# Kernel optimization log

Measured on AMD Instinct MI355X. Metric: run time of the kernel, lower is better.

The kernel has to match this reference:

```python
import jax, jax.numpy as jnp
import numpy as np
from jax import lax

PAD = 1  # 3x3 conv, stride 1, padding 1


def conv2d(x, w, b=None):
    # x: [B,C,H,W], w: [O,I,3,3]
    y = lax.conv_general_dilated(x, w, window_strides=(1, 1),
                                 padding=((PAD, PAD), (PAD, PAD)),
                                 dimension_numbers=("NCHW", "OIHW", "NCHW"))
    if b is not None:
        y = y + b[None, :, None, None]
    return y


def _bilinear(img, py, px):
    # img: [C,H,W]; py,px: [K,H,W] sampling coords (float). Zero padding outside.
    H, W = img.shape[1], img.shape[2]
    y0 = jnp.floor(py)
    x0 = jnp.floor(px)
    wy = py - y0  # [K,H,W]
    wx = px - x0
    y0i = y0.astype(jnp.int32)
    x0i = x0.astype(jnp.int32)

    def gather(yi, xi):
        valid = ((yi >= 0) & (yi < H) & (xi >= 0) & (xi < W)).astype(img.dtype)
        yc = jnp.clip(yi, 0, H - 1)
        xc = jnp.clip(xi, 0, W - 1)
        return img[:, yc, xc] * valid[None]  # [C,K,H,W]

    v00 = gather(y0i, x0i)
    v01 = gather(y0i, x0i + 1)
    v10 = gather(y0i + 1, x0i)
    v11 = gather(y0i + 1, x0i + 1)
    return (v00 * (1 - wy) * (1 - wx) + v01 * (1 - wy) * wx
            + v10 * wy * (1 - wx) + v11 * wy * wx)  # [C,K,H,W]


def reference(x, w_offset, b_offset, w_mask, b_mask, w_conv):
    B, C, H, W = x.shape
    K = 9  # 3x3 kernel taps
    offset = conv2d(x, w_offset, b_offset)              # [B,2K,H,W]
    mask = jax.nn.sigmoid(conv2d(x, w_mask, b_mask))    # [B,K,H,W]

    off = offset.reshape(B, K, 2, H, W)
    dy = off[:, :, 0]  # [B,K,H,W] (torchvision layout: y first)
    dx = off[:, :, 1]

    k = jnp.arange(K)
    ky = (k // 3).astype(x.dtype) - PAD  # tap row offset in {-1,0,1}
    kx = (k % 3).astype(x.dtype) - PAD
    ii = jnp.arange(H, dtype=x.dtype)
    jj = jnp.arange(W, dtype=x.dtype)

    py = ii[None, None, :, None] + ky[None, :, None, None] + dy  # [B,K,H,W]
    px = jj[None, None, None, :] + kx[None, :, None, None] + dx

    sampled = jax.vmap(_bilinear)(x, py, px)  # [B,C,K,H,W]
    sampled = sampled * mask[:, None]          # modulated deform-conv v2

    # weight [64,3,3,3] -> [O,C,K]; contract over C and kernel taps
    out = jnp.einsum('bckhw,ock->bohw', sampled, w_conv.reshape(w_conv.shape[0], C, K))
    return out


def setup_inputs() -> dict:
    key = jax.random.key(0)
    k = jax.random.split(key, 6)
    B, C, H, W = 16, 3, 256, 256
    return {
        'x': jax.random.normal(k[0], (B, C, H, W), jnp.float32),
        'w_offset': jax.random.normal(k[1], (18, 3, 3, 3), jnp.float32) * 0.1,
        'b_offset': jax.random.normal(k[2], (18,), jnp.float32) * 0.1,
        'w_mask': jax.random.normal(k[3], (9, 3, 3, 3), jnp.float32) * 0.1,
        'b_mask': jax.random.normal(k[4], (9,), jnp.float32) * 0.1,
        'w_conv': jax.random.normal(k[5], (64, 3, 3, 3), jnp.float32) * 0.1,
    }
```

## Files before the change

kernel.cpp:

```cpp
#include <hip/hip_runtime.h>
#include <hip/hip_bf16.h>

#define HH 256
#define WW 256
#define CC 3
#define KK 9
#define OC 64
#define KD 27
#define PSTS 40
#define MOFF 5120
#define MST 16
#define WRB 6144
#define XST (4 * WRB)
#define XSLOT 1024
#define ROWS 4
#define SLOTS 10

typedef __attribute__((ext_vector_type(8))) short bf16x8;
typedef __attribute__((ext_vector_type(4))) short s16x4;
typedef __attribute__((ext_vector_type(4))) float f32x4;
typedef __attribute__((ext_vector_type(2))) float f32x2;
typedef __attribute__((ext_vector_type(2))) unsigned int u32x2;

static __device__ __forceinline__ short f2bf(float f) {
    __hip_bfloat16 h = __float2bfloat16(f);
    return __builtin_bit_cast(short, h);
}
static __device__ __forceinline__ unsigned pack2(short a, short b) {
    return (unsigned)(unsigned short)a | ((unsigned)(unsigned short)b << 16);
}
static __device__ __forceinline__ float bf2f(unsigned w) {
    return __uint_as_float(w << 16);
}
static __device__ __forceinline__ float bfup(unsigned w) {
    return __uint_as_float(w & 0xffff0000u);
}

__global__ __launch_bounds__(256) void dcn_prep(
    const float* __restrict__ x,
    const float* __restrict__ w_offset, const float* __restrict__ b_offset,
    const float* __restrict__ w_mask,   const float* __restrict__ b_mask,
    const float* __restrict__ w_conv,
    short* __restrict__ xbf, short* __restrict__ wcf, char* __restrict__ wof,
    int npix)
{
    const int tid = threadIdx.x;
    if (blockIdx.x == gridDim.x - 1) {
        if (tid < 64) {
            const int fm = tid & 15, kc = tid >> 4;
#pragma unroll
            for (int t = 0; t < 4; ++t) {
                bf16x8 v;
#pragma unroll
                for (int e = 0; e < 8; ++e) {
                    int kd = kc * 8 + e;
                    v[e] = (kd < KD) ? f2bf(w_conv[(t * 16 + fm) * KD + kd]) : (short)0;
                }
                *(bf16x8*)(wcf + tid * 32 + t * 8) = v;
            }
#pragma unroll
            for (int t = 0; t < 2; ++t) {
                int ch = t * 16 + fm;
                bf16x8 vh, vl;
#pragma unroll
                for (int e = 0; e < 8; ++e) {
                    int kd = kc * 8 + e;
                    float val = 0.0f;
                    if (kd < KD) {
                        if (ch < 18) val = w_offset[ch * KD + kd];
                        else if (ch < KD) val = w_mask[(ch - 18) * KD + kd];
                    }
                    unsigned u = __float_as_uint(val);
                    vh[e] = (short)(u >> 16);
                    float d = val - __uint_as_float(u & 0xffff0000u);
                    vl[e] = (short)(__float_as_uint(d) >> 16);
                }
                *(bf16x8*)(wof + tid * 96 + t * 16) = vh;
                *(bf16x8*)(wof + tid * 96 + 32 + t * 16) = vl;
            }
#pragma unroll
            for (int t = 0; t < 2; ++t) {
                f32x4 cb;
#pragma unroll
                for (int r = 0; r < 4; ++r) {
                    int ch = t * 16 + kc * 4 + r;
                    float v = 0.0f;
                    if (ch < 18) v = b_offset[ch];
                    else if (ch < KD) v = b_mask[ch - 18];
                    cb[r] = v;
                }
                *(f32x4*)(wof + tid * 96 + 64 + t * 16) = cb;
            }
        }
        return;
    }

    const int p0 = (blockIdx.x * 256 + tid) * 4;
    if (p0 >= npix) return;
    const int bb = p0 >> 16;
    const int q  = p0 & 0xffff;
    const float* xb = x + (size_t)bb * (3 * 65536) + q;
    f32x4 r0 = *(const f32x4*)(xb);
    f32x4 r1 = *(const f32x4*)(xb + 65536);
    f32x4 r2 = *(const f32x4*)(xb + 131072);

    bf16x8 v0 = {f2bf(r0[0]), f2bf(r1[0]), f2bf(r2[0]), 0,
                 f2bf(r0[1]), f2bf(r1[1]), f2bf(r2[1]), 0};
    bf16x8 v1 = {f2bf(r0[2]), f2bf(r1[2]), f2bf(r2[2]), 0,
                 f2bf(r0[3]), f2bf(r1[3]), f2bf(r2[3]), 0};
    short* A = xbf + (size_t)p0 * 4;
    *(bf16x8*)A       = v0;
    *(bf16x8*)(A + 8) = v1;
}

__global__ __launch_bounds__(256) void dcn_main(
    const float* __restrict__ x,
    const short* __restrict__ xbf,
    const short* __restrict__ wcf,
    const char*  __restrict__ wof,
    float* __restrict__ out)
{
    __shared__ __align__(16) char LDSBUF[XST + SLOTS * XSLOT * 2];

    const int tid = threadIdx.x;
    const int j = tid;
    const int r0 = (blockIdx.x & 63) * ROWS;
    const int b = blockIdx.x >> 6;
    const int lane = tid & 63;
    const int wv = tid >> 6;
    const int fm = lane & 15;
    const int kc = lane >> 4;

    char* wbase = LDSBUF + wv * WRB;
    short* patchS = (short*)wbase;
    short* xs = (short*)(LDSBUF + XST);

    const float* xb = x + (size_t)b * (CC * HH * WW);
    const short* xrow = xbf + (size_t)b * (HH * WW * 4);

    {
        u32x2 st[SLOTS];
#pragma unroll
        for (int s = 0; s < SLOTS; ++s) {
            int gr = min(max(r0 - 3 + s, 0), HH - 1);
            st[s] = *(const u32x2*)(xrow + ((size_t)gr * WW + tid) * 4);
        }
#pragma unroll
        for (int s = 0; s < SLOTS; ++s) {
            *(u32x2*)(xs + s * XSLOT + tid * 4) = st[s];
        }
    }
    __syncthreads();

    const char* wl = wof + lane * 96;
    bf16x8 whi0 = *(const bf16x8*)(wl);
    bf16x8 whi1 = *(const bf16x8*)(wl + 16);
    bf16x8 wlo0 = *(const bf16x8*)(wl + 32);
    bf16x8 wlo1 = *(const bf16x8*)(wl + 48);
    f32x4 cb0 = *(const f32x4*)(wl + 64);
    f32x4 cb1 = *(const f32x4*)(wl + 80);
    bf16x8 afrag[4];
#pragma unroll
    for (int t2 = 0; t2 < 4; ++t2) afrag[t2] = *(const bf16x8*)(wcf + lane * 32 + t2 * 8);

    const float* x0p = xb;
    const float* x1p = xb + (size_t)HH * WW;
    const float* x2p = xb + (size_t)2 * HH * WW;

#pragma unroll 1
    for (int d = 0; d < ROWS; ++d) {
        const int ri = r0 + d;

        const bool yok0 = (ri - 1) >= 0, yok2 = (ri + 1) < HH;
        const bool xok0 = (j - 1) >= 0, xok2 = (j + 1) < WW;
        s16x4 pr[3][3];
#pragma unroll
        for (int p = 0; p < 3; ++p) {
#pragma unroll
            for (int q = 0; q < 3; ++q) {
                int xx = min(max(j + q - 1, 0), WW - 1);
                pr[p][q] = *(const s16x4*)(xs + (d + p + 2) * XSLOT + xx * 4);
            }
        }
        {
            short* rp = patchS + lane * PSTS;
#pragma unroll
            for (int o = 0; o < 4; ++o) {
                bf16x8 vh;
#pragma unroll
                for (int e = 0; e < 8; ++e) {
                    int kd = o * 8 + e;
                    if (kd < KD) {
                        int c = kd / 9, rem = kd - c * 9, p = rem / 3, q = rem - p * 3;
                        bool ok = (p == 0 ? yok0 : (p == 2 ? yok2 : true)) &&
                                  (q == 0 ? xok0 : (q == 2 ? xok2 : true));
                        vh[e] = ok ? pr[p][q][c] : (short)0;
                    } else {
                        vh[e] = (short)0;
                    }
                }
                *(bf16x8*)(rp + o * 8) = vh;
            }
        }

        f32x4 dacc[4][2];
#pragma unroll
        for (int g = 0; g < 4; ++g) {
            bf16x8 phi = *(const bf16x8*)(patchS + (g * 16 + fm) * PSTS + kc * 8);
            f32x4 a0 = __builtin_amdgcn_mfma_f32_16x16x32_bf16(whi0, phi, cb0, 0, 0, 0);
            a0 = __builtin_amdgcn_mfma_f32_16x16x32_bf16(wlo0, phi, a0, 0, 0, 0);
            f32x4 a1 = __builtin_amdgcn_mfma_f32_16x16x32_bf16(whi1, phi, cb1, 0, 0, 0);
            a1 = __builtin_amdgcn_mfma_f32_16x16x32_bf16(wlo1, phi, a1, 0, 0, 0);
            dacc[g][0] = a0;
            dacc[g][1] = a1;
        }
#pragma unroll
        for (int g = 0; g < 4; ++g) {
            int r = g * 16 + fm;
            char* dr = wbase + r * 80;
            char* mr = wbase + MOFF + r * MST;
            *(f32x4*)(dr + kc * 16) = dacc[g][0];
            f32x4 a1 = dacc[g][1];
            if (kc == 0) {
                *(f32x2*)(dr + 64) = (f32x2){a1[0], a1[1]};
                *(unsigned*)(dr + 72) = pack2(f2bf(a1[2]), f2bf(a1[3]));
            } else if (kc == 1) {
                *(unsigned*)(dr + 76) = pack2(f2bf(a1[0]), f2bf(a1[1]));
                *(unsigned*)(mr + 0) = pack2(f2bf(a1[2]), f2bf(a1[3]));
            } else if (kc == 2) {
                *(unsigned*)(mr + 4) = pack2(f2bf(a1[0]), f2bf(a1[1]));
                *(unsigned short*)(mr + 8) = (unsigned short)f2bf(a1[2]);
            }
        }

        const char* myD = wbase + lane * 80;
        f32x4 d03 = *(const f32x4*)(myD);
        f32x4 d47 = *(const f32x4*)(myD + 16);
        f32x4 d8b = *(const f32x4*)(myD + 32);
        f32x4 dcf = *(const f32x4*)(myD + 48);
        f32x2 d8p = *(const f32x2*)(myD + 64);
        u32x2 z03 = *(const u32x2*)(myD + 72);
        const char* myM = wbase + MOFF + lane * MST;
        u32x2 z47 = *(const u32x2*)(myM);
        unsigned z8w = *(const unsigned short*)(myM + 8);

        const float dyv[9] = {d03[0], d03[2], d47[0], d47[2], d8b[0], d8b[2], dcf[0], dcf[2], d8p[0]};
        const float dxv[9] = {d03[1], d03[3], d47[1], d47[3], d8b[1], d8b[3], dcf[1], dcf[3], d8p[1]};
        const float mzf[9] = {bf2f(z03.x), bfup(z03.x), bf2f(z03.y), bfup(z03.y),
                              bf2f(z47.x), bfup(z47.x), bf2f(z47.y), bfup(z47.y), bf2f(z8w)};

        float s27[KD];
#pragma unroll
        for (int k = 0; k < KK; ++k) {
            float dy = dyv[k], dx = dxv[k];
            float msk = 1.0f / (1.0f + __expf(-mzf[k]));

            float py = (float)(ri + (k / 3) - 1) + dy;
            float px = (float)(j + (k % 3) - 1) + dx;
            float y0f = floorf(py), x0f = floorf(px);
            float wy = py - y0f, wx = px - x0f;
            int y0 = (int)y0f, x0 = (int)x0f;
            int y1 = y0 + 1, x1 = x0 + 1;

            float w00 = (1.0f - wy) * (1.0f - wx);
            float w01 = (1.0f - wy) * wx;
            float w10 = wy * (1.0f - wx);
            float w11 = wy * wx;

            bool v0y = (unsigned)y0 < HH, v1y = (unsigned)y1 < HH;
            bool v0x = (unsigned)x0 < WW, v1x = (unsigned)x1 < WW;
            float f00 = (v0y && v0x) ? w00 : 0.0f;
            float f01 = (v0y && v1x) ? w01 : 0.0f;
            float f10 = (v1y && v0x) ? w10 : 0.0f;
            float f11 = (v1y && v1x) ? w11 : 0.0f;

            int y0c = min(max(y0, 0), HH - 1), y1c = min(max(y1, 0), HH - 1);
            int s0 = y0c - r0 + 3;
            int s1 = y1c - r0 + 3;
            float r0v_, r1v_, r2v_;
            if (__builtin_expect(__any(((unsigned)s0 > (SLOTS - 1)) ||
                                       ((unsigned)s1 > (SLOTS - 1))), 0)) {
                int x0c = min(max(x0, 0), WW - 1), x1c = min(max(x1, 0), WW - 1);
                int o00 = y0c * WW + x0c, o01 = y0c * WW + x1c;
                int o10 = y1c * WW + x0c, o11 = y1c * WW + x1c;
                r0v_ = x0p[o00] * f00 + x0p[o01] * f01 + x0p[o10] * f10 + x0p[o11] * f11;
                r1v_ = x1p[o00] * f00 + x1p[o01] * f01 + x1p[o10] * f10 + x1p[o11] * f11;
                r2v_ = x2p[o00] * f00 + x2p[o01] * f01 + x2p[o10] * f10 + x2p[o11] * f11;
            } else {
                int xl = min(max(x0, 0), WW - 2);
                bool sw = (x0 != xl);
                const short* p0 = xs + s0 * XSLOT + xl * 4;
                const short* p1 = xs + s1 * XSLOT + xl * 4;
                u32x2 lo0 = *(const u32x2*)p0;
                u32x2 hi0 = *(const u32x2*)(p0 + 4);
                u32x2 lo1 = *(const u32x2*)p1;
                u32x2 hi1 = *(const u32x2*)(p1 + 4);

                float a0 = sw ? f01 : f00, b0 = sw ? f00 : f01;
                float a1w = sw ? f11 : f10, b1w = sw ? f10 : f11;

                r0v_ = fmaf(bf2f(lo0.x), a0, fmaf(bf2f(hi0.x), b0,
                       fmaf(bf2f(lo1.x), a1w, bf2f(hi1.x) * b1w)));
                r1v_ = fmaf(bfup(lo0.x), a0, fmaf(bfup(hi0.x), b0,
                       fmaf(bfup(lo1.x), a1w, bfup(hi1.x) * b1w)));
                r2v_ = fmaf(bf2f(lo0.y), a0, fmaf(bf2f(hi0.y), b0,
                       fmaf(bf2f(lo1.y), a1w, bf2f(hi1.y) * b1w)));
            }
            s27[k]      = r0v_ * msk;
            s27[9 + k]  = r1v_ * msk;
            s27[18 + k] = r2v_ * msk;
        }

        {
            short* srow = patchS + lane * PSTS;
#pragma unroll
            for (int o = 0; o < 4; ++o) {
                bf16x8 v;
#pragma unroll
                for (int e = 0; e < 8; ++e) {
                    int kd = o * 8 + e;
                    v[e] = (kd < KD) ? f2bf(s27[kd]) : (short)0;
                }
                *(bf16x8*)(srow + o * 8) = v;
            }
        }

        float* obase = out + ((size_t)b * OC * HH + ri) * WW;
#pragma unroll
        for (int g = 0; g < 4; ++g) {
            bf16x8 sfrag = *(const bf16x8*)(patchS + (g * 16 + fm) * PSTS + kc * 8);
#pragma unroll
            for (int t2 = 0; t2 < 4; ++t2) {
                f32x4 acc = (f32x4){0.f, 0.f, 0.f, 0.f};
                acc = __builtin_amdgcn_mfma_f32_16x16x32_bf16(sfrag, afrag[t2], acc, 0, 0, 0);
                float* op = obase + (size_t)(t2 * 16 + fm) * (HH * WW) + (wv * 64 + g * 16 + kc * 4);
                *(f32x4*)op = acc;
            }
        }
    }
}

extern "C" void kernel_launch(void* const* d_in, const int* in_sizes, int n_in,
                              void* d_out, int out_size, void* d_ws, size_t ws_size,
                              hipStream_t stream) {
    const float* x        = (const float*)d_in[0];
    const float* w_offset = (const float*)d_in[1];
    const float* b_offset = (const float*)d_in[2];
    const float* w_mask   = (const float*)d_in[3];
    const float* b_mask   = (const float*)d_in[4];
    const float* w_conv   = (const float*)d_in[5];
    float* out = (float*)d_out;

    int B = in_sizes[0] / (CC * HH * WW);
    int npix = B * HH * WW;

    short* xbf = (short*)d_ws;
    short* wcf = (short*)((char*)d_ws + (size_t)npix * 8);
    char*  wof = (char*)d_ws + (size_t)npix * 8 + 4096;

    int nb = (npix + 1023) / 1024;
    hipLaunchKernelGGL(dcn_prep, dim3(nb + 1), dim3(256), 0, stream,
                       x, w_offset, b_offset, w_mask, b_mask, w_conv,
                       xbf, wcf, wof, npix);
    hipLaunchKernelGGL(dcn_main, dim3(B * (HH / ROWS)), dim3(256), 0, stream,
                       x, xbf, wcf, wof, out);
}
```

Measured before the change: 75.74 us.

## Shrink per-wave LDS, quantize mask to 8-bit, halve rows per block

```diff
diff --git a/kernel.cpp b/kernel.cpp
--- a/kernel.cpp
+++ b/kernel.cpp
@@ -8,19 +8,18 @@
 #define OC 64
 #define KD 27
 #define PSTS 40
-#define MOFF 5120
-#define MST 16
-#define WRB 6144
+#define WRB 5120
 #define XST (4 * WRB)
 #define XSLOT 1024
-#define ROWS 4
-#define SLOTS 10
+#define ROWS 2
+#define SLOTS 8
 
 typedef __attribute__((ext_vector_type(8))) short bf16x8;
 typedef __attribute__((ext_vector_type(4))) short s16x4;
 typedef __attribute__((ext_vector_type(4))) float f32x4;
 typedef __attribute__((ext_vector_type(2))) float f32x2;
 typedef __attribute__((ext_vector_type(2))) unsigned int u32x2;
+typedef __attribute__((ext_vector_type(4))) unsigned int u32x4;
 
 static __device__ __forceinline__ short f2bf(float f) {
     __hip_bfloat16 h = __float2bfloat16(f);
@@ -34,6 +33,10 @@
 }
 static __device__ __forceinline__ float bfup(unsigned w) {
     return __uint_as_float(w & 0xffff0000u);
+}
+static __device__ __forceinline__ unsigned q8(float z) {
+    float s = 1.0f / (1.0f + __expf(-z));
+    return (unsigned)__builtin_rintf(s * 255.0f);
 }
 
 __global__ __launch_bounds__(256) void dcn_prep(
@@ -113,7 +116,7 @@
     *(bf16x8*)(A + 8) = v1;
 }
 
-__global__ __launch_bounds__(256) void dcn_main(
+__global__ __launch_bounds__(256, 4) void dcn_main(
     const float* __restrict__ x,
     const short* __restrict__ xbf,
     const short* __restrict__ wcf,
@@ -124,8 +127,8 @@
 
     const int tid = threadIdx.x;
     const int j = tid;
-    const int r0 = (blockIdx.x & 63) * ROWS;
-    const int b = blockIdx.x >> 6;
+    const int r0 = (blockIdx.x & 127) * ROWS;
+    const int b = blockIdx.x >> 7;
     const int lane = tid & 63;
     const int wv = tid >> 6;
     const int fm = lane & 15;
@@ -218,18 +221,17 @@
         for (int g = 0; g < 4; ++g) {
             int r = g * 16 + fm;
             char* dr = wbase + r * 80;
-            char* mr = wbase + MOFF + r * MST;
             *(f32x4*)(dr + kc * 16) = dacc[g][0];
             f32x4 a1 = dacc[g][1];
             if (kc == 0) {
-                *(f32x2*)(dr + 64) = (f32x2){a1[0], a1[1]};
-                *(unsigned*)(dr + 72) = pack2(f2bf(a1[2]), f2bf(a1[3]));
+                *(unsigned*)(dr + 64) = pack2(f2bf(a1[0]), f2bf(a1[1]));
+                *(unsigned short*)(dr + 68) = (unsigned short)(q8(a1[2]) | (q8(a1[3]) << 8));
             } else if (kc == 1) {
-                *(unsigned*)(dr + 76) = pack2(f2bf(a1[0]), f2bf(a1[1]));
-                *(unsigned*)(mr + 0) = pack2(f2bf(a1[2]), f2bf(a1[3]));
+                *(unsigned short*)(dr + 70) = (unsigned short)(q8(a1[0]) | (q8(a1[1]) << 8));
+                *(unsigned short*)(dr + 72) = (unsigned short)(q8(a1[2]) | (q8(a1[3]) << 8));
             } else if (kc == 2) {
-                *(unsigned*)(mr + 4) = pack2(f2bf(a1[0]), f2bf(a1[1]));
-                *(unsigned short*)(mr + 8) = (unsigned short)f2bf(a1[2]);
+                *(unsigned short*)(dr + 74) = (unsigned short)(q8(a1[0]) | (q8(a1[1]) << 8));
+                *(unsigned short*)(dr + 76) = (unsigned short)q8(a1[2]);
             }
         }
 
@@ -238,22 +240,21 @@
         f32x4 d47 = *(const f32x4*)(myD + 16);
         f32x4 d8b = *(const f32x4*)(myD + 32);
         f32x4 dcf = *(const f32x4*)(myD + 48);
-        f32x2 d8p = *(const f32x2*)(myD + 64);
-        u32x2 z03 = *(const u32x2*)(myD + 72);
-        const char* myM = wbase + MOFF + lane * MST;
-        u32x2 z47 = *(const u32x2*)(myM);
-        unsigned z8w = *(const unsigned short*)(myM + 8);
-
-        const float dyv[9] = {d03[0], d03[2], d47[0], d47[2], d8b[0], d8b[2], dcf[0], dcf[2], d8p[0]};
-        const float dxv[9] = {d03[1], d03[3], d47[1], d47[3], d8b[1], d8b[3], dcf[1], dcf[3], d8p[1]};
-        const float mzf[9] = {bf2f(z03.x), bfup(z03.x), bf2f(z03.y), bfup(z03.y),
-                              bf2f(z47.x), bfup(z47.x), bf2f(z47.y), bfup(z47.y), bf2f(z8w)};
+        u32x4 tail = *(const u32x4*)(myD + 64);
+
+        const float dyv[9] = {d03[0], d03[2], d47[0], d47[2], d8b[0], d8b[2], dcf[0], dcf[2],
+                              bf2f(tail.x)};
+        const float dxv[9] = {d03[1], d03[3], d47[1], d47[3], d8b[1], d8b[3], dcf[1], dcf[3],
+                              bfup(tail.x)};
+        const unsigned mqv[9] = {tail.y & 255u, (tail.y >> 8) & 255u, (tail.y >> 16) & 255u,
+                                 tail.y >> 24, tail.z & 255u, (tail.z >> 8) & 255u,
+                                 (tail.z >> 16) & 255u, tail.z >> 24, tail.w & 255u};
 
         float s27[KD];
 #pragma unroll
         for (int k = 0; k < KK; ++k) {
             float dy = dyv[k], dx = dxv[k];
-            float msk = 1.0f / (1.0f + __expf(-mzf[k]));
+            float msk = (float)mqv[k] * (1.0f / 255.0f);
 
             float py = (float)(ri + (k / 3) - 1) + dy;
             float px = (float)(j + (k % 3) - 1) + dx;
```

After: 72.37 us (median of 2 runs). 4.4% less time.
